# Kernel tuning notes

Hardware: AMD Instinct MI355X
Metric: run time of the kernel (lower is better)

## Reference

```python
import jax, jax.numpy as jnp
import numpy as np

ROWS, COLS = 256, 256
IN_DIM, OUT_DIM = 64, 64
BATCH = 16
EPS_BN = 1e-5
EPS_DEG = 1e-5


def _stencil9(x):
    """Sum over the 3x3 neighborhood (8 neighbors + self) with zero padding.
    x: [..., R, C, F] -> same shape."""
    R, C = x.shape[-3], x.shape[-2]
    pad = [(0, 0)] * (x.ndim - 3) + [(1, 1), (1, 1), (0, 0)]
    xp = jnp.pad(x, pad)
    out = jnp.zeros_like(x)
    for di in range(3):
        for dj in range(3):
            out = out + xp[..., di:di + R, dj:dj + C, :]
    return out


def _deg_inv_sqrt(rows, cols, dtype):
    # D[i] = (#8-connected neighbors of i) + 1 (self loop) == 3x3 stencil of ones
    ones = jnp.ones((rows, cols, 1), dtype=dtype)
    D = _stencil9(ones)[..., 0]  # [R, C]
    return (D + EPS_DEG) ** -0.5


def setup_inputs() -> dict:
    key = jax.random.key(0)
    k1, k2 = jax.random.split(key)
    N = ROWS * COLS
    H = jax.random.normal(k1, (BATCH, N, IN_DIM), dtype=jnp.float32)
    # kaiming_uniform_ for relu: bound = sqrt(6 / fan_in)
    bound = np.sqrt(6.0 / IN_DIM)
    W = jax.random.uniform(k2, (IN_DIM, OUT_DIM), dtype=jnp.float32,
                           minval=-bound, maxval=bound)
    gamma = jnp.ones((OUT_DIM,), dtype=jnp.float32)
    beta = jnp.zeros((OUT_DIM,), dtype=jnp.float32)
    return {"H": H, "W": W, "gamma": gamma, "beta": beta}


def reference(H, W, gamma, beta):
    B, N, _ = H.shape
    # Linear: [B*N, in] @ [in, out]
    Ht = jnp.einsum('bni,io->bno', H, W)
    # BatchNorm1d (training mode: batch stats over B*N, biased variance)
    mean = jnp.mean(Ht, axis=(0, 1))
    var = jnp.var(Ht, axis=(0, 1))
    Ht = (Ht - mean) * jax.lax.rsqrt(var + EPS_BN) * gamma + beta
    # ReLU
    Ht = jax.nn.relu(Ht)
    # Normalized 8-connected grid aggregation: out = d_i * sum_{j in N(i) u {i}} d_j * h_j
    d = _deg_inv_sqrt(ROWS, COLS, Ht.dtype)[None, :, :, None]  # [1, R, C, 1]
    Hg = Ht.reshape(B, ROWS, COLS, OUT_DIM)
    Hagg = d * _stencil9(Hg * d)
    return Hagg.reshape(B, N, OUT_DIM)
```

## Files before the change

### kernel.cpp

```cpp
#include <hip/hip_runtime.h>
#include <hip/hip_bf16.h>

#define ROWS 256
#define COLS 256
#define BATCH 16
#define FDIM 64
#define NPIX (ROWS * COLS)
#define MTOT (BATCH * NPIX)

#define NB1 1024
#define K1_ITERS ((MTOT / 16) / (NB1 * 4))

typedef __attribute__((ext_vector_type(8))) short short8;
typedef __attribute__((ext_vector_type(4))) float floatx4;

__device__ __forceinline__ unsigned short f2bf(float f) {
    union { float f; unsigned int i; } v;
    v.f = f;
    unsigned int r = v.i + 0x7FFFu + ((v.i >> 16) & 1u);
    return (unsigned short)(r >> 16);
}
__device__ __forceinline__ float bf2f(unsigned short u) {
    union { unsigned int i; float f; } v;
    v.i = ((unsigned int)u) << 16;
    return v.f;
}
__device__ __forceinline__ short8 pack8(float4 x, float4 y) {
    short8 o;
    o[0] = (short)f2bf(x.x); o[1] = (short)f2bf(x.y);
    o[2] = (short)f2bf(x.z); o[3] = (short)f2bf(x.w);
    o[4] = (short)f2bf(y.x); o[5] = (short)f2bf(y.y);
    o[6] = (short)f2bf(y.z); o[7] = (short)f2bf(y.w);
    return o;
}
__device__ __forceinline__ float dinv(int r, int c) {
    int rv = 3 - (r == 0) - (r == ROWS - 1);
    int cv = 3 - (c == 0) - (c == COLS - 1);
    return rsqrtf((float)(rv * cv) + 1e-5f);
}

__device__ __forceinline__ void* pswz(void* Pbase, int pix, int fb) {
    unsigned off = ((unsigned)pix << 8) + (unsigned)fb;
    off ^= (((unsigned)pix >> 2) & 7u) << 5;
    return (char*)Pbase + off;
}

__global__ __launch_bounds__(256) void k1_stats(
    const float* __restrict__ H,
    const float* __restrict__ W,
    float* __restrict__ partials,
    float* __restrict__ stats,
    unsigned short* __restrict__ hbf)
{
    const int tid  = threadIdx.x;
    const int lane = tid & 63;
    const int wid  = tid >> 6;
    const int gw   = blockIdx.x * 4 + wid;
    const int n    = lane & 15;
    const int q    = lane >> 4;

    __shared__ float red[4][128];

    short8 bfrag[2][4];
    for (int kt = 0; kt < 2; ++kt)
        for (int nt = 0; nt < 4; ++nt)
            for (int j = 0; j < 8; ++j)
                bfrag[kt][nt][j] = (short)f2bf(W[(kt * 32 + q * 8 + j) * FDIM + nt * 16 + n]);

    float s[4]  = {0.f, 0.f, 0.f, 0.f};
    float s2[4] = {0.f, 0.f, 0.f, 0.f};

    #pragma unroll 2
    for (int it = 0; it < K1_ITERS; ++it) {
        const int t = gw + it * (NB1 * 4);
        const float4* ap = (const float4*)(H + ((size_t)t * 16 + n) * FDIM + q * 8);
        short8 a0 = pack8(ap[0], ap[1]);
        short8 a1 = pack8(ap[8], ap[9]);

        if (hbf) {
            short8* sp = (short8*)(hbf + ((size_t)t * 16 + n) * FDIM);
            sp[q]     = a0;
            sp[q + 4] = a1;
        }

        floatx4 acc[4] = {};
        for (int nt = 0; nt < 4; ++nt) {
            acc[nt] = __builtin_amdgcn_mfma_f32_16x16x32_bf16(a0, bfrag[0][nt], acc[nt], 0, 0, 0);
            acc[nt] = __builtin_amdgcn_mfma_f32_16x16x32_bf16(a1, bfrag[1][nt], acc[nt], 0, 0, 0);
        }
        for (int nt = 0; nt < 4; ++nt)
            for (int r = 0; r < 4; ++r) {
                float v = acc[nt][r];
                s[nt] += v;
                s2[nt] = fmaf(v, v, s2[nt]);
            }
    }

    for (int nt = 0; nt < 4; ++nt) {
        float a = s[nt], b = s2[nt];
        a += __shfl_xor(a, 16); b += __shfl_xor(b, 16);
        a += __shfl_xor(a, 32); b += __shfl_xor(b, 32);
        if (q == 0) {
            red[wid][nt * 16 + n]      = a;
            red[wid][64 + nt * 16 + n] = b;
        }
    }
    __syncthreads();

    if (tid < 128) {
        float tot = red[0][tid] + red[1][tid] + red[2][tid] + red[3][tid];
        if (partials) partials[(size_t)tid * NB1 + blockIdx.x] = tot;
        else          atomicAdd(&stats[tid], tot);
    }
}

__global__ __launch_bounds__(256) void k2_reduce(
    const float* __restrict__ partials,
    const float* __restrict__ gamma,
    const float* __restrict__ beta,
    float* __restrict__ ab)
{
    const int f   = blockIdx.x;
    const int tid = threadIdx.x;
    const float4* p0 = (const float4*)(partials + (size_t)f * NB1);
    const float4* p1 = (const float4*)(partials + (size_t)(f + 64) * NB1);
    float4 v0 = p0[tid];
    float4 v1 = p1[tid];
    float s0 = v0.x + v0.y + v0.z + v0.w;
    float s1 = v1.x + v1.y + v1.z + v1.w;
    for (int off = 1; off < 64; off <<= 1) {
        s0 += __shfl_xor(s0, off);
        s1 += __shfl_xor(s1, off);
    }
    __shared__ float r0[4], r1[4];
    const int wid = tid >> 6, lane = tid & 63;
    if (lane == 0) { r0[wid] = s0; r1[wid] = s1; }
    __syncthreads();
    if (tid == 0) {
        float S = r0[0] + r0[1] + r0[2] + r0[3];
        float Q = r1[0] + r1[1] + r1[2] + r1[3];
        const float inv_m = 1.0f / (float)MTOT;
        float mean = S * inv_m;
        float var  = Q * inv_m - mean * mean;
        float a = gamma[f] * rsqrtf(var + 1e-5f);
        ab[f]      = a;
        ab[64 + f] = beta[f] - mean * a;
    }
}

__global__ void k2_finalize(const float* __restrict__ stats,
                            const float* __restrict__ gamma,
                            const float* __restrict__ beta,
                            float* __restrict__ ab)
{
    int t = threadIdx.x;
    if (t < 64) {
        const float inv_m = 1.0f / (float)MTOT;
        float mean = stats[t] * inv_m;
        float var  = stats[64 + t] * inv_m - mean * mean;
        float a = gamma[t] * rsqrtf(var + 1e-5f);
        ab[t]      = a;
        ab[64 + t] = beta[t] - mean * a;
    }
}

#define TH 8
#define TW 16
#define IH (TH + 2)
#define IW (TW + 2)
#define NHALO (IH * IW)
#define NHPAD 192
#define NCHUNK 12

template <int USEHBF>
__global__ __launch_bounds__(256) void k3_fused(
    const float* __restrict__ H,
    const unsigned short* __restrict__ hbf,
    const float* __restrict__ W,
    const float* __restrict__ ab,
    float* __restrict__ out)
{
    __shared__ float P[NHPAD * FDIM];
    __shared__ float abv[2 * FDIM];
    __shared__ float djt[NHPAD];
    __shared__ int   gofft[NHPAD];

    const int tid  = threadIdx.x;
    const int lane = tid & 63;
    const int wid  = tid >> 6;
    const int n    = lane & 15;
    const int q    = lane >> 4;

    int bid = blockIdx.x;
    const int ct = bid & 15;  bid >>= 4;
    const int rt = bid & 31;  bid >>= 5;
    const int bb = bid;
    const int r0 = rt * TH, c0 = ct * TW;
    const size_t base = (size_t)bb * NPIX * FDIM;

    if (tid < 128) abv[tid] = ab[tid];
    if (tid < NHPAD) {
        int ri = tid / IW, ci = tid - ri * IW;
        int r = r0 - 1 + ri, c = c0 - 1 + ci;
        bool ok = (tid < NHALO) && ((unsigned)r < ROWS) && ((unsigned)c < COLS);
        djt[tid]   = ok ? dinv(r, c) : 0.f;
        gofft[tid] = ok ? (r * COLS + c) : -1;
    }

    short8 bfrag[2][4];
    #pragma unroll
    for (int kt = 0; kt < 2; ++kt)
        #pragma unroll
        for (int j = 0; j < 8; ++j) {
            const float4 wv = *(const float4*)&W[(kt * 32 + q * 8 + j) * FDIM + n * 4];
            bfrag[kt][0][j] = (short)f2bf(wv.x);
            bfrag[kt][1][j] = (short)f2bf(wv.y);
            bfrag[kt][2][j] = (short)f2bf(wv.z);
            bfrag[kt][3][j] = (short)f2bf(wv.w);
        }
    __syncthreads();

    const float4 av4 = *(const float4*)&abv[n * 4];
    const float4 bv4 = *(const float4*)&abv[64 + n * 4];

    #pragma unroll
    for (int cc = 0; cc < NCHUNK / 4; ++cc) {
        const int ch = cc * 4 + wid;
        const int p  = ch * 16 + n;
        const int go = gofft[p];
        short8 a0 = {}, a1 = {};
        if (USEHBF) {
            if (go >= 0) {
                const short8* ap = (const short8*)(hbf + base + (size_t)go * FDIM);
                a0 = ap[q];
                a1 = ap[q + 4];
            }
        } else {
            if (go >= 0) {
                const float4* apx = (const float4*)(H + base + (size_t)go * FDIM + q * 8);
                a0 = pack8(apx[0], apx[1]);
                a1 = pack8(apx[8], apx[9]);
            }
        }
        floatx4 acc[4] = {};
        #pragma unroll
        for (int nt = 0; nt < 4; ++nt) {
            acc[nt] = __builtin_amdgcn_mfma_f32_16x16x32_bf16(a0, bfrag[0][nt], acc[nt], 0, 0, 0);
            acc[nt] = __builtin_amdgcn_mfma_f32_16x16x32_bf16(a1, bfrag[1][nt], acc[nt], 0, 0, 0);
        }
        const int pb = ch * 16 + q * 4;
        const floatx4 dj4 = *(const floatx4*)&djt[pb];
        #pragma unroll
        for (int rr = 0; rr < 4; ++rr) {
            float4 w4;
            w4.x = fmaxf(fmaf(acc[0][rr], av4.x, bv4.x), 0.f) * dj4[rr];
            w4.y = fmaxf(fmaf(acc[1][rr], av4.y, bv4.y), 0.f) * dj4[rr];
            w4.z = fmaxf(fmaf(acc[2][rr], av4.z, bv4.z), 0.f) * dj4[rr];
            w4.w = fmaxf(fmaf(acc[3][rr], av4.w, bv4.w), 0.f) * dj4[rr];
            *(float4*)pswz(P, pb + rr, n * 16) = w4;
        }
    }
    __syncthreads();

    {
        const int fg  = tid & 7;
        const int ocg = (tid >> 3) & 3;
        const int orr = tid >> 5;
        const int hc0 = ocg * 4;
        const int fb  = fg * 32;

        float cs[3][8];
        #pragma unroll
        for (int ini = 0; ini < 2; ++ini) {
            const int p0 = (orr + 0) * IW + hc0 + ini;
            const int p1 = (orr + 1) * IW + hc0 + ini;
            const int p2 = (orr + 2) * IW + hc0 + ini;
            const float4 a0 = *(const float4*)pswz(P, p0, fb);
            const float4 a1 = *(const float4*)pswz(P, p0, fb + 16);
            const float4 b0 = *(const float4*)pswz(P, p1, fb);
            const float4 b1 = *(const float4*)pswz(P, p1, fb + 16);
            const float4 c0 = *(const float4*)pswz(P, p2, fb);
            const float4 c1 = *(const float4*)pswz(P, p2, fb + 16);
            cs[ini][0] = a0.x + b0.x + c0.x;
            cs[ini][1] = a0.y + b0.y + c0.y;
            cs[ini][2] = a0.z + b0.z + c0.z;
            cs[ini][3] = a0.w + b0.w + c0.w;
            cs[ini][4] = a1.x + b1.x + c1.x;
            cs[ini][5] = a1.y + b1.y + c1.y;
            cs[ini][6] = a1.z + b1.z + c1.z;
            cs[ini][7] = a1.w + b1.w + c1.w;
        }

        const int r = r0 + orr;
        float* orow = out + base + ((size_t)r * COLS + (c0 + hc0)) * FDIM + fg * 8;
        #pragma unroll
        for (int jj = 0; jj < 4; ++jj) {
            const int i0 = jj % 3, i1 = (jj + 1) % 3, i2 = (jj + 2) % 3;
            const int p0 = (orr + 0) * IW + hc0 + jj + 2;
            const int p1 = (orr + 1) * IW + hc0 + jj + 2;
            const int p2 = (orr + 2) * IW + hc0 + jj + 2;
            const float4 a0 = *(const float4*)pswz(P, p0, fb);
            const float4 a1 = *(const float4*)pswz(P, p0, fb + 16);
            const float4 b0 = *(const float4*)pswz(P, p1, fb);
            const float4 b1 = *(const float4*)pswz(P, p1, fb + 16);
            const float4 c0 = *(const float4*)pswz(P, p2, fb);
            const float4 c1 = *(const float4*)pswz(P, p2, fb + 16);
            cs[i2][0] = a0.x + b0.x + c0.x;
            cs[i2][1] = a0.y + b0.y + c0.y;
            cs[i2][2] = a0.z + b0.z + c0.z;
            cs[i2][3] = a0.w + b0.w + c0.w;
            cs[i2][4] = a1.x + b1.x + c1.x;
            cs[i2][5] = a1.y + b1.y + c1.y;
            cs[i2][6] = a1.z + b1.z + c1.z;
            cs[i2][7] = a1.w + b1.w + c1.w;
            const float d = djt[(orr + 1) * IW + hc0 + jj + 1];
            float4 o0, o1;
            o0.x = (cs[i0][0] + cs[i1][0] + cs[i2][0]) * d;
            o0.y = (cs[i0][1] + cs[i1][1] + cs[i2][1]) * d;
            o0.z = (cs[i0][2] + cs[i1][2] + cs[i2][2]) * d;
            o0.w = (cs[i0][3] + cs[i1][3] + cs[i2][3]) * d;
            o1.x = (cs[i0][4] + cs[i1][4] + cs[i2][4]) * d;
            o1.y = (cs[i0][5] + cs[i1][5] + cs[i2][5]) * d;
            o1.z = (cs[i0][6] + cs[i1][6] + cs[i2][6]) * d;
            o1.w = (cs[i0][7] + cs[i1][7] + cs[i2][7]) * d;
            float4* op = (float4*)(orow + (size_t)jj * FDIM);
            op[0] = o0; op[1] = o1;
        }
    }
}

extern "C" void kernel_launch(void* const* d_in, const int* in_sizes, int n_in,
                              void* d_out, int out_size, void* d_ws, size_t ws_size,
                              hipStream_t stream) {
    const float* H     = (const float*)d_in[0];
    const float* W     = (const float*)d_in[1];
    const float* gamma = (const float*)d_in[2];
    const float* beta  = (const float*)d_in[3];
    float* out = (float*)d_out;

    float* ab       = (float*)d_ws;
    float* stats    = ab + 128;
    float* partials = stats + 128;
    unsigned short* hbf = (unsigned short*)(partials + (size_t)128 * NB1);

    const size_t need_part = (size_t)(256 + 128 * NB1) * sizeof(float);
    const size_t need_full = need_part + (size_t)MTOT * FDIM * sizeof(unsigned short);

    if (ws_size >= need_full) {
        k1_stats<<<NB1, 256, 0, stream>>>(H, W, partials, nullptr, hbf);
        k2_reduce<<<64, 256, 0, stream>>>(partials, gamma, beta, ab);
        k3_fused<1><<<BATCH * 32 * 16, 256, 0, stream>>>(H, hbf, W, ab, out);
    } else if (ws_size >= need_part) {
        k1_stats<<<NB1, 256, 0, stream>>>(H, W, partials, nullptr, nullptr);
        k2_reduce<<<64, 256, 0, stream>>>(partials, gamma, beta, ab);
        k3_fused<0><<<BATCH * 32 * 16, 256, 0, stream>>>(H, nullptr, W, ab, out);
    } else {
        hipMemsetAsync(stats, 0, 128 * sizeof(float), stream);
        k1_stats<<<NB1, 256, 0, stream>>>(H, W, nullptr, stats, nullptr);
        k2_finalize<<<1, 64, 0, stream>>>(stats, gamma, beta, ab);
        k3_fused<0><<<BATCH * 32 * 16, 256, 0, stream>>>(H, nullptr, W, ab, out);
    }
}
```

Before: 533.2 us.

## Double stats blocks, use packed bf16 conversion, remap fused-kernel block order

Doubles the number of blocks in the stats pass (NB1 1024 to 2048), and the reduce kernel now loops over the extra partials. The hand-written bf16 rounding is replaced with the packed float2-to-bfloat162 intrinsic. The fused kernel's block index is permuted so consecutive hardware block IDs spread across eight strided groups, likely to match the XCD round-robin dispatch for better L2 locality. These are three unrelated tweaks that trade more partials traffic and a different tile order for more parallelism and cheaper conversion.

After: 537.2 us. About the same (+0.8%).

```diff
diff --git a/kernel.cpp b/kernel.cpp
--- a/kernel.cpp
+++ b/kernel.cpp
@@ -8,7 +8,7 @@
 #define NPIX (ROWS * COLS)
 #define MTOT (BATCH * NPIX)
 
-#define NB1 1024
+#define NB1 2048
 #define K1_ITERS ((MTOT / 16) / (NB1 * 4))
 
 typedef __attribute__((ext_vector_type(8))) short short8;
@@ -25,13 +25,19 @@
     v.i = ((unsigned int)u) << 16;
     return v.f;
 }
+__device__ __forceinline__ unsigned int cvtpk(float lo, float hi) {
+    __hip_bfloat162 h = __float22bfloat162_rn(make_float2(lo, hi));
+    union { __hip_bfloat162 h; unsigned int u; } v;
+    v.h = h;
+    return v.u;
+}
 __device__ __forceinline__ short8 pack8(float4 x, float4 y) {
-    short8 o;
-    o[0] = (short)f2bf(x.x); o[1] = (short)f2bf(x.y);
-    o[2] = (short)f2bf(x.z); o[3] = (short)f2bf(x.w);
-    o[4] = (short)f2bf(y.x); o[5] = (short)f2bf(y.y);
-    o[6] = (short)f2bf(y.z); o[7] = (short)f2bf(y.w);
-    return o;
+    union { short8 s; unsigned int u[4]; } o;
+    o.u[0] = cvtpk(x.x, x.y);
+    o.u[1] = cvtpk(x.z, x.w);
+    o.u[2] = cvtpk(y.x, y.y);
+    o.u[3] = cvtpk(y.z, y.w);
+    return o.s;
 }
 __device__ __forceinline__ float dinv(int r, int c) {
     int rv = 3 - (r == 0) - (r == ROWS - 1);
@@ -124,10 +130,14 @@
     const int tid = threadIdx.x;
     const float4* p0 = (const float4*)(partials + (size_t)f * NB1);
     const float4* p1 = (const float4*)(partials + (size_t)(f + 64) * NB1);
-    float4 v0 = p0[tid];
-    float4 v1 = p1[tid];
-    float s0 = v0.x + v0.y + v0.z + v0.w;
-    float s1 = v1.x + v1.y + v1.z + v1.w;
+    float s0 = 0.f, s1 = 0.f;
+    #pragma unroll
+    for (int i = 0; i < NB1 / 1024; ++i) {
+        float4 v0 = p0[tid + i * 256];
+        float4 v1 = p1[tid + i * 256];
+        s0 += v0.x + v0.y + v0.z + v0.w;
+        s1 += v1.x + v1.y + v1.z + v1.w;
+    }
     for (int off = 1; off < 64; off <<= 1) {
         s0 += __shfl_xor(s0, off);
         s1 += __shfl_xor(s1, off);
@@ -191,7 +201,7 @@
     const int n    = lane & 15;
     const int q    = lane >> 4;
 
-    int bid = blockIdx.x;
+    int bid = (blockIdx.x & 7) * ((BATCH * 32 * 16) >> 3) + (blockIdx.x >> 3);
     const int ct = bid & 15;  bid >>= 4;
     const int rt = bid & 31;  bid >>= 5;
     const int bb = bid;
```
